# Optimization experiments

Measured on AMD Instinct MI355X. Metric: run time of the kernel, lower is better.

## Reference

```python
import jax, jax.numpy as jnp
import numpy as np

HEADS = 16  # per module init; all heads share the same weights -> identical outputs


def setup_inputs() -> dict:
    key = jax.random.key(0)
    k1, k2, k3, k4 = jax.random.split(key, 4)
    B, S, E, HD = 8, 2048, 1024, 64  # embed_size=1024, heads=16, head_dim=64
    x = jax.random.normal(k1, (B, S, E), dtype=jnp.float32)
    Wq = jax.random.normal(k2, (HD, E), dtype=jnp.float32) * (E ** -0.5)
    Wk = jax.random.normal(k3, (HD, E), dtype=jnp.float32) * (E ** -0.5)
    Wv = jax.random.normal(k4, (HD, E), dtype=jnp.float32) * (E ** -0.5)
    return {"x": x, "Wq": Wq, "Wk": Wk, "Wv": Wv}


def reference(x, Wq, Wk, Wv):
    # Linear(embed, head_dim, bias=False): y = x @ W.T
    q = jnp.einsum('bse,de->bsd', x, Wq)  # [B,S,64]
    k = jnp.einsum('bse,de->bsd', x, Wk)
    v = jnp.einsum('bse,de->bsd', x, Wv)
    # scores [b, i(query), k(key)] -- NO scaling (scaled_factor unused in source)
    scores = jnp.einsum('bij,bkj->bik', q, k)
    # nn.Softmax(dim=1): normalize over the QUERY axis (axis=1), faithful quirk
    attn = jax.nn.softmax(scores, axis=1)
    out = jnp.matmul(attn, v)  # [B,S,64]
    # Per-head loop reuses identical weights -> concat == tile across heads
    return jnp.tile(out, (1, 1, HEADS))  # [B,S,1024]
```

## Files before the change

### kernel.cpp

```cpp
#include <hip/hip_runtime.h>

#define BATCH 8
#define SEQ   2048
#define EMB   1024
#define HD    64
#define HEADS 16
#define BS    (BATCH * SEQ)
#define LOG2E 1.4426950408889634f

typedef _Float16 half8 __attribute__((ext_vector_type(8)));
typedef _Float16 half4 __attribute__((ext_vector_type(4)));
typedef float    f32x4 __attribute__((ext_vector_type(4)));

__device__ __forceinline__ float fexp2(float x) {
#if __has_builtin(__builtin_amdgcn_exp2f)
    return __builtin_amdgcn_exp2f(x);
#else
    return exp2f(x);
#endif
}

__device__ __forceinline__ float frcp(float x) {
#if __has_builtin(__builtin_amdgcn_rcpf)
    return __builtin_amdgcn_rcpf(x);
#else
    return 1.0f / x;
#endif
}

__device__ __forceinline__ void dma16(void* lds_base, const void* gsrc) {
    __builtin_amdgcn_global_load_lds(
        (const __attribute__((address_space(1))) unsigned int*)gsrc,
        (__attribute__((address_space(3))) unsigned int*)lds_base, 16, 0, 0);
}

__global__ __launch_bounds__(256) void wcvt_kernel(
    const float* __restrict__ Wq, const float* __restrict__ Wk,
    const float* __restrict__ Wv, _Float16* __restrict__ Wh)
{
    const int m = blockIdx.y;
    const float* src = (m == 0) ? Wq : (m == 1) ? Wk : Wv;
    const float scale = (m == 0) ? LOG2E : 1.0f;
    const int idx = (blockIdx.x * 256 + threadIdx.x) * 8;
    float4 f0 = *(const float4*)(src + idx);
    float4 f1 = *(const float4*)(src + idx + 4);
    half8 h;
    h[0] = (_Float16)(f0.x * scale); h[1] = (_Float16)(f0.y * scale);
    h[2] = (_Float16)(f0.z * scale); h[3] = (_Float16)(f0.w * scale);
    h[4] = (_Float16)(f1.x * scale); h[5] = (_Float16)(f1.y * scale);
    h[6] = (_Float16)(f1.z * scale); h[7] = (_Float16)(f1.w * scale);
    *(half8*)(Wh + (size_t)m * 65536 + idx) = h;
}

__global__ __launch_bounds__(512) void qkv_kernel(
    const float* __restrict__ x, const _Float16* __restrict__ Wh,
    _Float16* __restrict__ qh, _Float16* __restrict__ kh, _Float16* __restrict__ vpt)
{
    __shared__ __align__(16) char arena[65536];
    const int t = threadIdx.x, lane = t & 63, wave = t >> 6;
    const int l15 = lane & 15, quad = lane >> 4;
    const int strip = wave & 1, grp = wave >> 1;
    const int row0 = blockIdx.x * 32;

    auto issue = [&](int buf, int k0) {
        #pragma unroll
        for (int jj = 0; jj < 4; ++jj) {
            const int j = wave * 4 + jj;
            if (j < 8) {
                const int row = j * 4 + (lane >> 4);
                const int logi = (lane & 15) ^ (row & 15);
                dma16((float*)(arena + buf * 8192) + j * 256,
                      x + (size_t)(row0 + row) * EMB + k0 + logi * 4);
            } else {
                const int jw = j - 8;
                const int dd = jw * 8 + (lane >> 3);
                const int logi = (lane & 7) ^ (dd & 7);
                dma16((_Float16*)(arena + 16384 + buf * 24576) + jw * 512,
                      Wh + (size_t)(dd >> 6) * 65536 + (size_t)(dd & 63) * EMB
                         + k0 + logi * 8);
            }
        }
    };

    issue(0, 0);
    __syncthreads();

    f32x4 acc[3] = {};
    const int xrow = strip * 16 + l15;
    for (int it = 0; it < 16; ++it) {
        const int buf = it & 1;
        if (it + 1 < 16) issue(buf ^ 1, (it + 1) * 64);
        const float* xb = (const float*)(arena + buf * 8192);
        const _Float16* wb = (const _Float16*)(arena + 16384 + buf * 24576);
        half8 a[2];
        #pragma unroll
        for (int kc = 0; kc < 2; ++kc) {
            const int s0 = kc * 8 + quad * 2;
            f32x4 u0 = *(const f32x4*)(xb + xrow * 64 + ((s0    ) ^ (l15 & 15)) * 4);
            f32x4 u1 = *(const f32x4*)(xb + xrow * 64 + ((s0 + 1) ^ (l15 & 15)) * 4);
            a[kc][0] = (_Float16)u0[0]; a[kc][1] = (_Float16)u0[1];
            a[kc][2] = (_Float16)u0[2]; a[kc][3] = (_Float16)u0[3];
            a[kc][4] = (_Float16)u1[0]; a[kc][5] = (_Float16)u1[1];
            a[kc][6] = (_Float16)u1[2]; a[kc][7] = (_Float16)u1[3];
        }
        #pragma unroll
        for (int j = 0; j < 3; ++j) {
            const int dd = (grp * 3 + j) * 16 + l15;
            #pragma unroll
            for (int kc = 0; kc < 2; ++kc) {
                half8 bfr = *(const half8*)(wb + dd * 64
                              + (((kc * 4 + quad) ^ (l15 & 7)) * 8));
                acc[j] = __builtin_amdgcn_mfma_f32_16x16x32_f16(a[kc], bfr, acc[j], 0, 0, 0);
            }
        }
        __syncthreads();
    }

    #pragma unroll
    for (int j = 0; j < 3; ++j) {
        const int c = grp * 3 + j, m = c >> 2, n = c & 3;
        if (m < 2) {
            _Float16* __restrict__ dst = (m == 0) ? qh : kh;
            #pragma unroll
            for (int r = 0; r < 4; ++r)
                dst[(size_t)(row0 + strip * 16 + quad * 4 + r) * HD + n * 16 + l15] =
                    (_Float16)acc[j][r];
        } else {
            const int rg = row0 + strip * 16 + quad * 4;
            const int b = rg >> 11, s = rg & 2047;
            half4 h;
            h[0] = (_Float16)acc[j][0]; h[1] = (_Float16)acc[j][1];
            h[2] = (_Float16)acc[j][2]; h[3] = (_Float16)acc[j][3];
            *(half4*)(vpt + ((size_t)b * HD + n * 16 + l15) * SEQ + s) = h;
        }
    }
}

__global__ __launch_bounds__(256) void stats_kernel(
    const _Float16* __restrict__ qh, const _Float16* __restrict__ kh,
    float* __restrict__ l_part)
{
    __shared__ __align__(16) char arena[16384];
    __shared__ float red[4][64];
    const int t = threadIdx.x, lane = t & 63, wave = t >> 6;
    const int l15 = lane & 15, quad = lane >> 4;
    const int b = blockIdx.y, c0 = blockIdx.x * 64, z = blockIdx.z;
    const int qbase = z * 1024;

    half8 ka[4][2];
    #pragma unroll
    for (int kt = 0; kt < 4; ++kt) {
        const _Float16* kp = kh + ((size_t)b * SEQ + c0 + kt * 16 + l15) * HD + quad * 8;
        ka[kt][0] = *(const half8*)(kp);
        ka[kt][1] = *(const half8*)(kp + 32);
    }

    auto issue = [&](int buf, int q0) {
        #pragma unroll
        for (int jj = 0; jj < 2; ++jj) {
            const int j = wave * 2 + jj;
            const int qq = j * 8 + (lane >> 3);
            const int logi = (lane & 7) ^ (qq & 7);
            dma16((_Float16*)(arena + buf * 8192) + j * 512,
                  qh + ((size_t)b * SEQ + q0 + qq) * HD + logi * 8);
        }
    };

    issue(0, qbase);
    __syncthreads();

    float csum[4][4] = {};
    const int qrow = wave * 16 + l15;
    for (int it = 0; it < 16; ++it) {
        const int buf = it & 1;
        if (it + 1 < 16) issue(buf ^ 1, qbase + (it + 1) * 64);
        const _Float16* qb = (const _Float16*)(arena + buf * 8192);
        half8 bq0 = *(const half8*)(qb + qrow * 64 + (((quad    ) ^ (l15 & 7)) * 8));
        half8 bq1 = *(const half8*)(qb + qrow * 64 + (((4 + quad) ^ (l15 & 7)) * 8));
        #pragma unroll
        for (int kt = 0; kt < 4; ++kt) {
            f32x4 s = {};
            s = __builtin_amdgcn_mfma_f32_16x16x32_f16(ka[kt][0], bq0, s, 0, 0, 0);
            s = __builtin_amdgcn_mfma_f32_16x16x32_f16(ka[kt][1], bq1, s, 0, 0, 0);
            #pragma unroll
            for (int r = 0; r < 4; ++r)
                csum[kt][r] += fexp2(s[r]);
        }
        __syncthreads();
    }
    #pragma unroll
    for (int kt = 0; kt < 4; ++kt)
        #pragma unroll
        for (int r = 0; r < 4; ++r) {
            csum[kt][r] += __shfl_xor(csum[kt][r], 1);
            csum[kt][r] += __shfl_xor(csum[kt][r], 2);
            csum[kt][r] += __shfl_xor(csum[kt][r], 4);
            csum[kt][r] += __shfl_xor(csum[kt][r], 8);
        }
    if (l15 == 0) {
        #pragma unroll
        for (int kt = 0; kt < 4; ++kt)
            #pragma unroll
            for (int r = 0; r < 4; ++r)
                red[wave][kt * 16 + quad * 4 + r] = csum[kt][r];
    }
    __syncthreads();
    if (t < 64)
        l_part[(size_t)z * BS + (size_t)b * SEQ + c0 + t] =
            red[0][t] + red[1][t] + red[2][t] + red[3][t];
}

__global__ __launch_bounds__(256) void out_kernel(
    const _Float16* __restrict__ qh, const _Float16* __restrict__ kh,
    const _Float16* __restrict__ vpt, const float* __restrict__ l_part,
    float* __restrict__ opart)
{
    __shared__ __align__(16) char arena[42496];
    const int t = threadIdx.x, lane = t & 63, wave = t >> 6;
    const int l15 = lane & 15, quad = lane >> 4;
    const int b = blockIdx.y, r0 = blockIdx.x * 64, z = blockIdx.z;
    const int kbase = z * 1024;

    half8 aq[2];
    {
        const _Float16* qp = qh + ((size_t)b * SEQ + r0 + wave * 16 + l15) * HD + quad * 8;
        aq[0] = *(const half8*)(qp);
        aq[1] = *(const half8*)(qp + 32);
    }

    auto issue = [&](int buf, int c0) {
        #pragma unroll
        for (int jj = 0; jj < 4; ++jj) {
            if (wave < 2) {
                const int j = wave * 4 + jj;
                const int key = j * 8 + (lane >> 3);
                const int logi = (lane & 7) ^ (key & 7);
                dma16((_Float16*)(arena + buf * 8192) + j * 512,
                      kh + ((size_t)b * SEQ + c0 + key) * HD + logi * 8);
            } else {
                const int j = (wave - 2) * 4 + jj;
                const int d = j * 8 + (lane >> 3);
                const int logi = (lane & 7) ^ (d & 7);
                dma16((_Float16*)(arena + 16384 + buf * 8192) + j * 512,
                      vpt + ((size_t)b * HD + d) * SEQ + c0 + logi * 8);
            }
        }
    };

    const float* lp = l_part + (size_t)b * SEQ;

    issue(0, kbase);
    __syncthreads();

    _Float16* psb = (_Float16*)(arena + 32768) + wave * 1216;
    f32x4 oacc[4] = {};
    for (int it = 0; it < 16; ++it) {
        const int buf = it & 1;
        if (it + 1 < 16) issue(buf ^ 1, kbase + (it + 1) * 64);
        const _Float16* kb = (const _Float16*)(arena + buf * 8192);
        const _Float16* vb = (const _Float16*)(arena + 16384 + buf * 8192);

        #pragma unroll
        for (int ct = 0; ct < 4; ++ct) {
            const int key = ct * 16 + l15;
            f32x4 s = {};
            half8 kf0 = *(const half8*)(kb + key * 64 + (((quad    ) ^ (l15 & 7)) * 8));
            half8 kf1 = *(const half8*)(kb + key * 64 + (((4 + quad) ^ (l15 & 7)) * 8));
            s = __builtin_amdgcn_mfma_f32_16x16x32_f16(aq[0], kf0, s, 0, 0, 0);
            s = __builtin_amdgcn_mfma_f32_16x16x32_f16(aq[1], kf1, s, 0, 0, 0);
            const int kg = kbase + it * 64 + key;
            const float li = frcp(lp[kg] + lp[BS + kg]);
            #pragma unroll
            for (int r = 0; r < 4; ++r)
                psb[(quad * 4 + r) * 76 + ct * 16 + l15] =
                    (_Float16)(fexp2(s[r]) * li);
        }
        half8 paA = *(const half8*)(psb + l15 * 76 + quad * 8);
        half8 paB = *(const half8*)(psb + l15 * 76 + 32 + quad * 8);
        #pragma unroll
        for (int n = 0; n < 4; ++n) {
            const int d = n * 16 + l15;
            half8 vfA = *(const half8*)(vb + d * 64 + (((quad    ) ^ (l15 & 7)) * 8));
            half8 vfB = *(const half8*)(vb + d * 64 + (((4 + quad) ^ (l15 & 7)) * 8));
            oacc[n] = __builtin_amdgcn_mfma_f32_16x16x32_f16(paA, vfA, oacc[n], 0, 0, 0);
            oacc[n] = __builtin_amdgcn_mfma_f32_16x16x32_f16(paB, vfB, oacc[n], 0, 0, 0);
        }
        __syncthreads();
    }

    #pragma unroll
    for (int n = 0; n < 4; ++n)
        #pragma unroll
        for (int r = 0; r < 4; ++r) {
            const int row = r0 + wave * 16 + quad * 4 + r;
            opart[(size_t)z * ((size_t)BS * HD)
                  + ((size_t)b * SEQ + row) * HD + n * 16 + l15] = oacc[n][r];
        }
}

__global__ __launch_bounds__(256) void bcast_kernel(
    const float* __restrict__ opart, float* __restrict__ out)
{
    const int row = blockIdx.x;
    const int t = threadIdx.x;
    const int d = (t * 4) & 63;
    const float* o0 = opart + (size_t)row * HD + d;
    const float* o1 = o0 + (size_t)BS * HD;
    float4 a = *(const float4*)o0;
    float4 c = *(const float4*)o1;
    float4 s;
    s.x = a.x + c.x; s.y = a.y + c.y; s.z = a.z + c.z; s.w = a.w + c.w;
    *(float4*)(out + (size_t)row * (HD * HEADS) + t * 4) = s;
}

extern "C" void kernel_launch(void* const* d_in, const int* in_sizes, int n_in,
                              void* d_out, int out_size, void* d_ws, size_t ws_size,
                              hipStream_t stream)
{
    const float* x  = (const float*)d_in[0];
    const float* Wq = (const float*)d_in[1];
    const float* Wk = (const float*)d_in[2];
    const float* Wv = (const float*)d_in[3];
    float* out = (float*)d_out;

    const size_t N = (size_t)BATCH * SEQ * HD;
    _Float16* qh  = (_Float16*)d_ws;
    _Float16* kh  = qh + N;
    _Float16* vpt = kh + N;
    _Float16* Wh  = vpt + N;
    float* l_part = (float*)(Wh + 196608);
    float* opart  = l_part + 2 * BS;

    wcvt_kernel <<<dim3(32, 3),    256, 0, stream>>>(Wq, Wk, Wv, Wh);
    qkv_kernel  <<<dim3(512),      512, 0, stream>>>(x, Wh, qh, kh, vpt);
    stats_kernel<<<dim3(32, 8, 2), 256, 0, stream>>>(qh, kh, l_part);
    out_kernel  <<<dim3(32, 8, 2), 256, 0, stream>>>(qh, kh, vpt, l_part, opart);
    bcast_kernel<<<dim3(BS),       256, 0, stream>>>(opart, out);
}
```

Measured before the change: 174.8 us.

## Prefetch two tiles ahead with explicit vmcnt waits and stage softmax denominators in LDS

In the projection, column-sum and output kernels, the double-buffered loops now issue loads two iterations ahead. They replace __syncthreads with s_barrier plus explicit s_waitcnt vmcnt, so outstanding global-to-LDS DMAs can overlap compute instead of being fully drained at every barrier. The output kernel also precomputes the reciprocal column sums for its 1024-key range into LDS once, removing per-tile global loads and rcp from the inner loop. This costs about 4 KB more LDS per block and depends on hand-written waitcnt values staying correct; a wrong count would cause a race.

```diff
diff --git a/kernel.cpp b/kernel.cpp
--- a/kernel.cpp
+++ b/kernel.cpp
@@ -33,6 +33,10 @@
         (const __attribute__((address_space(1))) unsigned int*)gsrc,
         (__attribute__((address_space(3))) unsigned int*)lds_base, 16, 0, 0);
 }
+
+#define VMCNT(N) asm volatile("s_waitcnt vmcnt(" #N ")" ::: "memory")
+#define LGKM0()  asm volatile("s_waitcnt lgkmcnt(0)" ::: "memory")
+#define SBAR()   __builtin_amdgcn_s_barrier()
 
 __global__ __launch_bounds__(256) void wcvt_kernel(
     const float* __restrict__ Wq, const float* __restrict__ Wk,
@@ -83,13 +87,14 @@
     };
 
     issue(0, 0);
-    __syncthreads();
+    issue(1, 64);
+    VMCNT(4);
+    SBAR();
 
     f32x4 acc[3] = {};
     const int xrow = strip * 16 + l15;
     for (int it = 0; it < 16; ++it) {
         const int buf = it & 1;
-        if (it + 1 < 16) issue(buf ^ 1, (it + 1) * 64);
         const float* xb = (const float*)(arena + buf * 8192);
         const _Float16* wb = (const _Float16*)(arena + 16384 + buf * 24576);
         half8 a[2];
@@ -113,7 +118,14 @@
                 acc[j] = __builtin_amdgcn_mfma_f32_16x16x32_f16(a[kc], bfr, acc[j], 0, 0, 0);
             }
         }
-        __syncthreads();
+        SBAR();
+        if (it + 2 < 16) {
+            issue(buf, (it + 2) * 64);
+            VMCNT(4);
+        } else {
+            VMCNT(0);
+        }
+        SBAR();
     }
 
     #pragma unroll
@@ -167,13 +179,14 @@
     };
 
     issue(0, qbase);
-    __syncthreads();
+    issue(1, qbase + 64);
+    VMCNT(2);
+    SBAR();
 
     float csum[4][4] = {};
     const int qrow = wave * 16 + l15;
     for (int it = 0; it < 16; ++it) {
         const int buf = it & 1;
-        if (it + 1 < 16) issue(buf ^ 1, qbase + (it + 1) * 64);
         const _Float16* qb = (const _Float16*)(arena + buf * 8192);
         half8 bq0 = *(const half8*)(qb + qrow * 64 + (((quad    ) ^ (l15 & 7)) * 8));
         half8 bq1 = *(const half8*)(qb + qrow * 64 + (((4 + quad) ^ (l15 & 7)) * 8));
@@ -186,7 +199,14 @@
             for (int r = 0; r < 4; ++r)
                 csum[kt][r] += fexp2(s[r]);
         }
-        __syncthreads();
+        SBAR();
+        if (it + 2 < 16) {
+            issue(buf, qbase + (it + 2) * 64);
+            VMCNT(2);
+        } else {
+            VMCNT(0);
+        }
+        SBAR();
     }
     #pragma unroll
     for (int kt = 0; kt < 4; ++kt)
@@ -215,7 +235,7 @@
     const _Float16* __restrict__ vpt, const float* __restrict__ l_part,
     float* __restrict__ opart)
 {
-    __shared__ __align__(16) char arena[42496];
+    __shared__ __align__(16) char arena[46592];
     const int t = threadIdx.x, lane = t & 63, wave = t >> 6;
     const int l15 = lane & 15, quad = lane >> 4;
     const int b = blockIdx.y, r0 = blockIdx.x * 64, z = blockIdx.z;
@@ -227,6 +247,11 @@
         aq[0] = *(const half8*)(qp);
         aq[1] = *(const half8*)(qp + 32);
     }
+
+    const float* lp = l_part + (size_t)b * SEQ;
+    float* ls = (float*)(arena + 42496);
+    for (int i = t; i < 1024; i += 256)
+        ls[i] = frcp(lp[kbase + i] + lp[BS + kbase + i]);
 
     auto issue = [&](int buf, int c0) {
         #pragma unroll
@@ -247,16 +272,16 @@
         }
     };
 
-    const float* lp = l_part + (size_t)b * SEQ;
-
     issue(0, kbase);
-    __syncthreads();
+    issue(1, kbase + 64);
+    LGKM0();
+    VMCNT(4);
+    SBAR();
 
     _Float16* psb = (_Float16*)(arena + 32768) + wave * 1216;
     f32x4 oacc[4] = {};
     for (int it = 0; it < 16; ++it) {
         const int buf = it & 1;
-        if (it + 1 < 16) issue(buf ^ 1, kbase + (it + 1) * 64);
         const _Float16* kb = (const _Float16*)(arena + buf * 8192);
         const _Float16* vb = (const _Float16*)(arena + 16384 + buf * 8192);
 
@@ -268,8 +293,7 @@
             half8 kf1 = *(const half8*)(kb + key * 64 + (((4 + quad) ^ (l15 & 7)) * 8));
             s = __builtin_amdgcn_mfma_f32_16x16x32_f16(aq[0], kf0, s, 0, 0, 0);
             s = __builtin_amdgcn_mfma_f32_16x16x32_f16(aq[1], kf1, s, 0, 0, 0);
-            const int kg = kbase + it * 64 + key;
-            const float li = frcp(lp[kg] + lp[BS + kg]);
+            const float li = ls[it * 64 + key];
             #pragma unroll
             for (int r = 0; r < 4; ++r)
                 psb[(quad * 4 + r) * 76 + ct * 16 + l15] =
@@ -285,7 +309,14 @@
             oacc[n] = __builtin_amdgcn_mfma_f32_16x16x32_f16(paA, vfA, oacc[n], 0, 0, 0);
             oacc[n] = __builtin_amdgcn_mfma_f32_16x16x32_f16(paB, vfB, oacc[n], 0, 0, 0);
         }
-        __syncthreads();
+        SBAR();
+        if (it + 2 < 16) {
+            issue(buf, kbase + (it + 2) * 64);
+            VMCNT(4);
+        } else {
+            VMCNT(0);
+        }
+        SBAR();
     }
 
     #pragma unroll
```

New measurement: 174.8 us. No clear change (-0.0%).

## Load QKV weights directly into registers and retile stats/out kernels

Applied to the files above, without the earlier changes.

The QKV projection kernel now streams weights straight from global memory into registers with double-buffered register sets, and stages only x through a smaller shared-memory buffer. The stats kernel covers 128 keys per block and splits the query range four ways, so l_part grows to four partial sums. The out kernel uses 512 threads and 128 query rows per block, and precomputes the reciprocal column sums into shared memory once per block instead of reading them per key tile. The aim is lower LDS traffic and less repeated l_part work, traded against more register pressure and a different occupancy profile.

```diff
diff --git a/kernel.cpp b/kernel.cpp
--- a/kernel.cpp
+++ b/kernel.cpp
@@ -56,48 +56,39 @@
     const float* __restrict__ x, const _Float16* __restrict__ Wh,
     _Float16* __restrict__ qh, _Float16* __restrict__ kh, _Float16* __restrict__ vpt)
 {
-    __shared__ __align__(16) char arena[65536];
+    __shared__ __align__(16) char arena[16384];
     const int t = threadIdx.x, lane = t & 63, wave = t >> 6;
     const int l15 = lane & 15, quad = lane >> 4;
     const int strip = wave & 1, grp = wave >> 1;
     const int row0 = blockIdx.x * 32;
 
-    auto issue = [&](int buf, int k0) {
-        #pragma unroll
-        for (int jj = 0; jj < 4; ++jj) {
-            const int j = wave * 4 + jj;
-            if (j < 8) {
-                const int row = j * 4 + (lane >> 4);
-                const int logi = (lane & 15) ^ (row & 15);
-                dma16((float*)(arena + buf * 8192) + j * 256,
-                      x + (size_t)(row0 + row) * EMB + k0 + logi * 4);
-            } else {
-                const int jw = j - 8;
-                const int dd = jw * 8 + (lane >> 3);
-                const int logi = (lane & 7) ^ (dd & 7);
-                dma16((_Float16*)(arena + 16384 + buf * 24576) + jw * 512,
-                      Wh + (size_t)(dd >> 6) * 65536 + (size_t)(dd & 63) * EMB
-                         + k0 + logi * 8);
-            }
-        }
-    };
-
-    issue(0, 0);
-    __syncthreads();
+    auto issueX = [&](int buf, int k0) {
+        const int row = wave * 4 + (lane >> 4);
+        const int logi = (lane & 15) ^ (row & 15);
+        dma16((float*)(arena + buf * 8192) + wave * 256,
+              x + (size_t)(row0 + row) * EMB + k0 + logi * 4);
+    };
+    auto loadW = [&](int k0, half8 (&w)[3][2]) {
+        #pragma unroll
+        for (int j = 0; j < 3; ++j) {
+            const int g = (grp * 3 + j) * 16 + l15;
+            const _Float16* wp = Wh + (size_t)(g >> 6) * 65536
+                               + (size_t)(g & 63) * EMB + k0 + quad * 8;
+            w[j][0] = *(const half8*)(wp);
+            w[j][1] = *(const half8*)(wp + 32);
+        }
+    };
 
     f32x4 acc[3] = {};
     const int xrow = strip * 16 + l15;
-    for (int it = 0; it < 16; ++it) {
-        const int buf = it & 1;
-        if (it + 1 < 16) issue(buf ^ 1, (it + 1) * 64);
+    auto step = [&](int buf, const half8 (&w)[3][2]) {
         const float* xb = (const float*)(arena + buf * 8192);
-        const _Float16* wb = (const _Float16*)(arena + 16384 + buf * 24576);
         half8 a[2];
         #pragma unroll
         for (int kc = 0; kc < 2; ++kc) {
             const int s0 = kc * 8 + quad * 2;
-            f32x4 u0 = *(const f32x4*)(xb + xrow * 64 + ((s0    ) ^ (l15 & 15)) * 4);
-            f32x4 u1 = *(const f32x4*)(xb + xrow * 64 + ((s0 + 1) ^ (l15 & 15)) * 4);
+            f32x4 u0 = *(const f32x4*)(xb + xrow * 64 + ((s0    ) ^ l15) * 4);
+            f32x4 u1 = *(const f32x4*)(xb + xrow * 64 + ((s0 + 1) ^ l15) * 4);
             a[kc][0] = (_Float16)u0[0]; a[kc][1] = (_Float16)u0[1];
             a[kc][2] = (_Float16)u0[2]; a[kc][3] = (_Float16)u0[3];
             a[kc][4] = (_Float16)u1[0]; a[kc][5] = (_Float16)u1[1];
@@ -105,14 +96,22 @@
         }
         #pragma unroll
         for (int j = 0; j < 3; ++j) {
-            const int dd = (grp * 3 + j) * 16 + l15;
-            #pragma unroll
-            for (int kc = 0; kc < 2; ++kc) {
-                half8 bfr = *(const half8*)(wb + dd * 64
-                              + (((kc * 4 + quad) ^ (l15 & 7)) * 8));
-                acc[j] = __builtin_amdgcn_mfma_f32_16x16x32_f16(a[kc], bfr, acc[j], 0, 0, 0);
-            }
-        }
+            acc[j] = __builtin_amdgcn_mfma_f32_16x16x32_f16(a[0], w[j][0], acc[j], 0, 0, 0);
+            acc[j] = __builtin_amdgcn_mfma_f32_16x16x32_f16(a[1], w[j][1], acc[j], 0, 0, 0);
+        }
+    };
+
+    half8 wA[3][2], wB[3][2];
+    issueX(0, 0);
+    loadW(0, wA);
+    __syncthreads();
+    for (int it = 0; it < 16; it += 2) {
+        issueX(1, (it + 1) * 64);
+        loadW((it + 1) * 64, wB);
+        step(0, wA);
+        __syncthreads();
+        if (it + 2 < 16) { issueX(0, (it + 2) * 64); loadW((it + 2) * 64, wA); }
+        step(1, wB);
         __syncthreads();
     }
 
@@ -141,15 +140,15 @@
     float* __restrict__ l_part)
 {
     __shared__ __align__(16) char arena[16384];
-    __shared__ float red[4][64];
+    __shared__ float red[4][128];
     const int t = threadIdx.x, lane = t & 63, wave = t >> 6;
     const int l15 = lane & 15, quad = lane >> 4;
-    const int b = blockIdx.y, c0 = blockIdx.x * 64, z = blockIdx.z;
-    const int qbase = z * 1024;
-
-    half8 ka[4][2];
+    const int b = blockIdx.y, c0 = blockIdx.x * 128, z = blockIdx.z;
+    const int qbase = z * 512;
+
+    half8 ka[8][2];
     #pragma unroll
-    for (int kt = 0; kt < 4; ++kt) {
+    for (int kt = 0; kt < 8; ++kt) {
         const _Float16* kp = kh + ((size_t)b * SEQ + c0 + kt * 16 + l15) * HD + quad * 8;
         ka[kt][0] = *(const half8*)(kp);
         ka[kt][1] = *(const half8*)(kp + 32);
@@ -162,23 +161,23 @@
             const int qq = j * 8 + (lane >> 3);
             const int logi = (lane & 7) ^ (qq & 7);
             dma16((_Float16*)(arena + buf * 8192) + j * 512,
-                  qh + ((size_t)b * SEQ + q0 + qq) * HD + logi * 8);
-        }
-    };
-
-    issue(0, qbase);
+                  qh + ((size_t)b * SEQ + qbase + q0 + qq) * HD + logi * 8);
+        }
+    };
+
+    issue(0, 0);
     __syncthreads();
 
-    float csum[4][4] = {};
+    float csum[8][4] = {};
     const int qrow = wave * 16 + l15;
-    for (int it = 0; it < 16; ++it) {
+    for (int it = 0; it < 8; ++it) {
         const int buf = it & 1;
-        if (it + 1 < 16) issue(buf ^ 1, qbase + (it + 1) * 64);
+        if (it + 1 < 8) issue(buf ^ 1, (it + 1) * 64);
         const _Float16* qb = (const _Float16*)(arena + buf * 8192);
         half8 bq0 = *(const half8*)(qb + qrow * 64 + (((quad    ) ^ (l15 & 7)) * 8));
         half8 bq1 = *(const half8*)(qb + qrow * 64 + (((4 + quad) ^ (l15 & 7)) * 8));
         #pragma unroll
-        for (int kt = 0; kt < 4; ++kt) {
+        for (int kt = 0; kt < 8; ++kt) {
             f32x4 s = {};
             s = __builtin_amdgcn_mfma_f32_16x16x32_f16(ka[kt][0], bq0, s, 0, 0, 0);
             s = __builtin_amdgcn_mfma_f32_16x16x32_f16(ka[kt][1], bq1, s, 0, 0, 0);
@@ -189,7 +188,7 @@
         __syncthreads();
     }
     #pragma unroll
-    for (int kt = 0; kt < 4; ++kt)
+    for (int kt = 0; kt < 8; ++kt)
         #pragma unroll
         for (int r = 0; r < 4; ++r) {
             csum[kt][r] += __shfl_xor(csum[kt][r], 1);
@@ -199,26 +198,26 @@
         }
     if (l15 == 0) {
         #pragma unroll
-        for (int kt = 0; kt < 4; ++kt)
+        for (int kt = 0; kt < 8; ++kt)
             #pragma unroll
             for (int r = 0; r < 4; ++r)
                 red[wave][kt * 16 + quad * 4 + r] = csum[kt][r];
     }
     __syncthreads();
-    if (t < 64)
+    if (t < 128)
         l_part[(size_t)z * BS + (size_t)b * SEQ + c0 + t] =
             red[0][t] + red[1][t] + red[2][t] + red[3][t];
 }
 
-__global__ __launch_bounds__(256) void out_kernel(
+__global__ __launch_bounds__(512) void out_kernel(
     const _Float16* __restrict__ qh, const _Float16* __restrict__ kh,
     const _Float16* __restrict__ vpt, const float* __restrict__ l_part,
     float* __restrict__ opart)
 {
-    __shared__ __align__(16) char arena[42496];
+    __shared__ __align__(16) char arena[56320];
     const int t = threadIdx.x, lane = t & 63, wave = t >> 6;
     const int l15 = lane & 15, quad = lane >> 4;
-    const int b = blockIdx.y, r0 = blockIdx.x * 64, z = blockIdx.z;
+    const int b = blockIdx.y, r0 = blockIdx.x * 128, z = blockIdx.z;
     const int kbase = z * 1024;
 
     half8 aq[2];
@@ -228,17 +227,24 @@
         aq[1] = *(const half8*)(qp + 32);
     }
 
+    const float* lp = l_part + (size_t)b * SEQ;
+    float* ls = (float*)(arena + 52224);
+    for (int i = t; i < 1024; i += 512) {
+        const int kg = kbase + i;
+        ls[i] = frcp((lp[kg] + lp[BS + kg]) + (lp[2 * BS + kg] + lp[3 * BS + kg]));
+    }
+
     auto issue = [&](int buf, int c0) {
         #pragma unroll
-        for (int jj = 0; jj < 4; ++jj) {
-            if (wave < 2) {
-                const int j = wave * 4 + jj;
+        for (int jj = 0; jj < 2; ++jj) {
+            if (wave < 4) {
+                const int j = wave * 2 + jj;
                 const int key = j * 8 + (lane >> 3);
                 const int logi = (lane & 7) ^ (key & 7);
                 dma16((_Float16*)(arena + buf * 8192) + j * 512,
                       kh + ((size_t)b * SEQ + c0 + key) * HD + logi * 8);
             } else {
-                const int j = (wave - 2) * 4 + jj;
+                const int j = (wave - 4) * 2 + jj;
                 const int d = j * 8 + (lane >> 3);
                 const int logi = (lane & 7) ^ (d & 7);
                 dma16((_Float16*)(arena + 16384 + buf * 8192) + j * 512,
@@ -246,8 +252,6 @@
             }
         }
     };
-
-    const float* lp = l_part + (size_t)b * SEQ;
 
     issue(0, kbase);
     __syncthreads();
@@ -268,8 +272,7 @@
             half8 kf1 = *(const half8*)(kb + key * 64 + (((4 + quad) ^ (l15 & 7)) * 8));
             s = __builtin_amdgcn_mfma_f32_16x16x32_f16(aq[0], kf0, s, 0, 0, 0);
             s = __builtin_amdgcn_mfma_f32_16x16x32_f16(aq[1], kf1, s, 0, 0, 0);
-            const int kg = kbase + it * 64 + key;
-            const float li = frcp(lp[kg] + lp[BS + kg]);
+            const float li = ls[it * 64 + key];
             #pragma unroll
             for (int r = 0; r < 4; ++r)
                 psb[(quad * 4 + r) * 76 + ct * 16 + l15] =
@@ -329,11 +332,11 @@
     _Float16* vpt = kh + N;
     _Float16* Wh  = vpt + N;
     float* l_part = (float*)(Wh + 196608);
-    float* opart  = l_part + 2 * BS;
+    float* opart  = l_part + 4 * BS;
 
     wcvt_kernel <<<dim3(32, 3),    256, 0, stream>>>(Wq, Wk, Wv, Wh);
     qkv_kernel  <<<dim3(512),      512, 0, stream>>>(x, Wh, qh, kh, vpt);
-    stats_kernel<<<dim3(32, 8, 2), 256, 0, stream>>>(qh, kh, l_part);
-    out_kernel  <<<dim3(32, 8, 2), 256, 0, stream>>>(qh, kh, vpt, l_part, opart);
+    stats_kernel<<<dim3(16, 8, 4), 256, 0, stream>>>(qh, kh, l_part);
+    out_kernel  <<<dim3(16, 8, 2), 512, 0, stream>>>(qh, kh, vpt, l_part, opart);
     bcast_kernel<<<dim3(BS),       256, 0, stream>>>(opart, out);
 }
```

Result: slower. 201.2 us (+15.1%).

## Load pre-swizzled QKV weights directly into registers instead of LDS staging

Applied to the files above, without the earlier changes.

The weight conversion kernel now writes fp16 weights in an MFMA-fragment-ordered layout, so each lane in the QKV projection kernel can read its B operand with a contiguous 16-byte global load. Only the x tile is staged in LDS, and weight fragments are double-buffered in registers across an unrolled two-step loop. This shrinks LDS use from 64KB to 16KB, which may allow more blocks per CU, and removes the weight DMA and LDS reads. The cost is more VGPRs and global/L2 loads of weights that are no longer shared through LDS across waves.

```diff
diff --git a/kernel.cpp b/kernel.cpp
--- a/kernel.cpp
+++ b/kernel.cpp
@@ -49,55 +49,51 @@
     h[2] = (_Float16)(f0.z * scale); h[3] = (_Float16)(f0.w * scale);
     h[4] = (_Float16)(f1.x * scale); h[5] = (_Float16)(f1.y * scale);
     h[6] = (_Float16)(f1.z * scale); h[7] = (_Float16)(f1.w * scale);
-    *(half8*)(Wh + (size_t)m * 65536 + idx) = h;
+    const int d = idx >> 10, k = idx & 1023;
+    const int dd = m * 64 + d;
+    const size_t off = ((((size_t)(dd >> 4) * 16 + (k >> 6)) * 8
+                         + ((k & 63) >> 3)) * 16 + (dd & 15)) * 8;
+    *(half8*)(Wh + off) = h;
 }
 
 __global__ __launch_bounds__(512) void qkv_kernel(
     const float* __restrict__ x, const _Float16* __restrict__ Wh,
     _Float16* __restrict__ qh, _Float16* __restrict__ kh, _Float16* __restrict__ vpt)
 {
-    __shared__ __align__(16) char arena[65536];
+    __shared__ __align__(16) char arena[16384];
     const int t = threadIdx.x, lane = t & 63, wave = t >> 6;
     const int l15 = lane & 15, quad = lane >> 4;
     const int strip = wave & 1, grp = wave >> 1;
     const int row0 = blockIdx.x * 32;
 
-    auto issue = [&](int buf, int k0) {
-        #pragma unroll
-        for (int jj = 0; jj < 4; ++jj) {
-            const int j = wave * 4 + jj;
-            if (j < 8) {
-                const int row = j * 4 + (lane >> 4);
-                const int logi = (lane & 15) ^ (row & 15);
-                dma16((float*)(arena + buf * 8192) + j * 256,
-                      x + (size_t)(row0 + row) * EMB + k0 + logi * 4);
-            } else {
-                const int jw = j - 8;
-                const int dd = jw * 8 + (lane >> 3);
-                const int logi = (lane & 7) ^ (dd & 7);
-                dma16((_Float16*)(arena + 16384 + buf * 24576) + jw * 512,
-                      Wh + (size_t)(dd >> 6) * 65536 + (size_t)(dd & 63) * EMB
-                         + k0 + logi * 8);
-            }
-        }
-    };
-
-    issue(0, 0);
-    __syncthreads();
+    auto issueX = [&](int buf, int k0) {
+        const int row = wave * 4 + (lane >> 4);
+        const int logi = (lane & 15) ^ (row & 15);
+        dma16((float*)(arena + buf * 8192) + wave * 256,
+              x + (size_t)(row0 + row) * EMB + k0 + logi * 4);
+    };
+    auto loadW = [&](int k0, half8 (&w)[3][2]) {
+        const int kchunk = k0 >> 6;
+        #pragma unroll
+        for (int j = 0; j < 3; ++j) {
+            const int tile = grp * 3 + j;
+            const _Float16* wp = Wh
+                + (((size_t)tile * 16 + kchunk) * 8) * 128;
+            w[j][0] = *(const half8*)(wp + ((quad    ) * 16 + l15) * 8);
+            w[j][1] = *(const half8*)(wp + ((4 + quad) * 16 + l15) * 8);
+        }
+    };
 
     f32x4 acc[3] = {};
     const int xrow = strip * 16 + l15;
-    for (int it = 0; it < 16; ++it) {
-        const int buf = it & 1;
-        if (it + 1 < 16) issue(buf ^ 1, (it + 1) * 64);
+    auto step = [&](int buf, const half8 (&w)[3][2]) {
         const float* xb = (const float*)(arena + buf * 8192);
-        const _Float16* wb = (const _Float16*)(arena + 16384 + buf * 24576);
         half8 a[2];
         #pragma unroll
         for (int kc = 0; kc < 2; ++kc) {
             const int s0 = kc * 8 + quad * 2;
-            f32x4 u0 = *(const f32x4*)(xb + xrow * 64 + ((s0    ) ^ (l15 & 15)) * 4);
-            f32x4 u1 = *(const f32x4*)(xb + xrow * 64 + ((s0 + 1) ^ (l15 & 15)) * 4);
+            f32x4 u0 = *(const f32x4*)(xb + xrow * 64 + ((s0    ) ^ l15) * 4);
+            f32x4 u1 = *(const f32x4*)(xb + xrow * 64 + ((s0 + 1) ^ l15) * 4);
             a[kc][0] = (_Float16)u0[0]; a[kc][1] = (_Float16)u0[1];
             a[kc][2] = (_Float16)u0[2]; a[kc][3] = (_Float16)u0[3];
             a[kc][4] = (_Float16)u1[0]; a[kc][5] = (_Float16)u1[1];
@@ -105,14 +101,22 @@
         }
         #pragma unroll
         for (int j = 0; j < 3; ++j) {
-            const int dd = (grp * 3 + j) * 16 + l15;
-            #pragma unroll
-            for (int kc = 0; kc < 2; ++kc) {
-                half8 bfr = *(const half8*)(wb + dd * 64
-                              + (((kc * 4 + quad) ^ (l15 & 7)) * 8));
-                acc[j] = __builtin_amdgcn_mfma_f32_16x16x32_f16(a[kc], bfr, acc[j], 0, 0, 0);
-            }
-        }
+            acc[j] = __builtin_amdgcn_mfma_f32_16x16x32_f16(a[0], w[j][0], acc[j], 0, 0, 0);
+            acc[j] = __builtin_amdgcn_mfma_f32_16x16x32_f16(a[1], w[j][1], acc[j], 0, 0, 0);
+        }
+    };
+
+    half8 wA[3][2], wB[3][2];
+    issueX(0, 0);
+    loadW(0, wA);
+    __syncthreads();
+    for (int it = 0; it < 16; it += 2) {
+        issueX(1, (it + 1) * 64);
+        loadW((it + 1) * 64, wB);
+        step(0, wA);
+        __syncthreads();
+        if (it + 2 < 16) { issueX(0, (it + 2) * 64); loadW((it + 2) * 64, wA); }
+        step(1, wB);
         __syncthreads();
     }
 
```

Measured after the change: 180.8 us. 1.03x slower.
